# Optimization experiments

Measured on AMD Instinct MI355X. Metric: run time of the kernel, lower is better.

The kernel has to match this reference:

```python
import jax, jax.numpy as jnp
import numpy as np

N_AUTHOR, N_PAPER = 20000, 40000
E = 400000
IN_DIM, HIDDEN, HEADS, NUM_CLASSES, NUM_LAYERS = 128, 128, 8, 16, 2
DIM = HIDDEN // HEADS
NEG_SLOPE = 0.2
AUTHOR_RAW = 64


def setup_inputs() -> dict:
    key = jax.random.key(0)
    ks = jax.random.split(key, 16)
    s = 0.05
    return {
        'x_author': jax.random.normal(ks[0], (N_AUTHOR, AUTHOR_RAW), jnp.float32),
        'x_paper': jax.random.normal(ks[1], (N_PAPER, IN_DIM), jnp.float32),
        'Wa': jax.random.normal(ks[2], (AUTHOR_RAW, IN_DIM), jnp.float32) * s,
        'proj_w': jax.random.normal(ks[3], (NUM_LAYERS, 2, IN_DIM, HIDDEN), jnp.float32) * s,
        'proj_b': jnp.zeros((NUM_LAYERS, 2, HIDDEN), jnp.float32),
        'att_src': jax.random.normal(ks[4], (NUM_LAYERS, 3, HEADS, DIM), jnp.float32) * s,
        'att_dst': jax.random.normal(ks[5], (NUM_LAYERS, 3, HEADS, DIM), jnp.float32) * s,
        'klin_w': jax.random.normal(ks[6], (NUM_LAYERS, HIDDEN, HIDDEN), jnp.float32) * s,
        'klin_b': jnp.zeros((NUM_LAYERS, HIDDEN), jnp.float32),
        'q': jax.random.normal(ks[7], (NUM_LAYERS, HIDDEN), jnp.float32) * s,
        'lin_w': jax.random.normal(ks[8], (HIDDEN, NUM_CLASSES), jnp.float32) * s,
        'lin_b': jnp.zeros((NUM_CLASSES,), jnp.float32),
        'ei_writes': jnp.stack([jax.random.randint(ks[9], (E,), 0, N_AUTHOR),
                                jax.random.randint(ks[10], (E,), 0, N_PAPER)]),
        'ei_written_by': jnp.stack([jax.random.randint(ks[11], (E,), 0, N_PAPER),
                                    jax.random.randint(ks[12], (E,), 0, N_AUTHOR)]),
        'ei_cites': jnp.stack([jax.random.randint(ks[13], (E,), 0, N_PAPER),
                               jax.random.randint(ks[14], (E,), 0, N_PAPER)]),
    }


def _segment_softmax(scores, seg, num_segments):
    # scores: [E, H]; softmax over edges sharing a destination node.
    m = jax.ops.segment_max(scores, seg, num_segments=num_segments)
    m = jnp.where(jnp.isfinite(m), m, 0.0)
    e = jnp.exp(scores - m[seg])
    denom = jax.ops.segment_sum(e, seg, num_segments=num_segments)
    return e / (denom[seg] + 1e-16)


def _han_forward(x_author, x_paper, Wa, proj_w, proj_b, att_src, att_dst,
                 klin_w, klin_b, q, lin_w, lin_b,
                 ei_writes, ei_written_by, ei_cites):
    # Type-alignment projector (author: 64 -> 128, no bias; paper: Identity)
    x = {'author': x_author @ Wa, 'paper': x_paper}
    nsize = {'author': N_AUTHOR, 'paper': N_PAPER}
    ntidx = {'author': 0, 'paper': 1}
    edge_types = [('author', 'paper', ei_writes),
                  ('paper', 'author', ei_written_by),
                  ('paper', 'paper', ei_cites)]
    for l in range(NUM_LAYERS):
        # Per-node-type projection -> [N, H, D]
        xh = {nt: (x[nt] @ proj_w[l, ntidx[nt]] + proj_b[l, ntidx[nt]]).reshape(-1, HEADS, DIM)
              for nt in x}
        outs = {'author': [], 'paper': []}
        for e_id, (src, dst, ei) in enumerate(edge_types):
            a_src = (xh[src] * att_src[l, e_id]).sum(-1)  # [N_src, H]
            a_dst = (xh[dst] * att_dst[l, e_id]).sum(-1)  # [N_dst, H]
            si, di = ei[0], ei[1]
            alpha = a_src[si] + a_dst[di]                 # [E, H]
            alpha = jnp.where(alpha >= 0, alpha, NEG_SLOPE * alpha)  # leaky_relu
            alpha = _segment_softmax(alpha, di, nsize[dst])
            # attention dropout omitted (eval mode)
            msg = (xh[src][si] * alpha[:, :, None]).reshape(-1, HIDDEN)  # [E, HIDDEN]
            agg = jax.ops.segment_sum(msg, di, num_segments=nsize[dst])
            outs[dst].append(jax.nn.relu(agg))
        # Semantic-level attention over metapath embeddings per node type
        newx = {}
        for nt, xs in outs.items():
            stk = jnp.stack(xs)  # [M, N, F]
            score = (q[l] * jnp.tanh(stk @ klin_w[l] + klin_b[l]).mean(axis=1)).sum(-1)  # [M]
            attn = jax.nn.softmax(score)
            newx[nt] = (attn[:, None, None] * stk).sum(0)
        x = newx
        if l < NUM_LAYERS - 1:
            x = {nt: jax.nn.relu(v) for nt, v in x.items()}
            # feature dropout omitted (eval mode)
    return x['paper'] @ lin_w + lin_b  # [N_PAPER, NUM_CLASSES]


def reference(x_author, x_paper, Wa, proj_w, proj_b, att_src, att_dst,
              klin_w, klin_b, q, lin_w, lin_b,
              ei_writes, ei_written_by, ei_cites):
    return _han_forward(x_author, x_paper, Wa, proj_w, proj_b, att_src, att_dst,
                        klin_w, klin_b, q, lin_w, lin_b,
                        ei_writes, ei_written_by, ei_cites)
```

## Files before the change

### kernel.cpp

```cpp
#include <hip/hip_runtime.h>
#include <hip/hip_bf16.h>

typedef __hip_bfloat16 bf16;
typedef __hip_bfloat162 bf162;

#define N_AUTHOR 20000
#define N_PAPER  40000
#define NEDGE    400000
#define HID      128
#define HEADS    8
#define DIMH     16
#define NCLS     16

typedef short short4v __attribute__((ext_vector_type(4)));
typedef short short8v __attribute__((ext_vector_type(8)));
typedef float f32x4   __attribute__((ext_vector_type(4)));

__device__ __forceinline__ bf162 mk2(float a, float b){
    bf162 r; r.x = __float2bfloat16(a); r.y = __float2bfloat16(b); return r;
}

__device__ __forceinline__ float fast_tanh(float x){
    x = fminf(fmaxf(x, -15.f), 15.f);
    float e = __expf(2.f * x);
    return (e - 1.f) / (e + 1.f);
}

template<int KDIM, int EPI>
__device__ __forceinline__ void bgemm_body(
    const bf16* __restrict__ A, const bf16* __restrict__ Wt, const float* __restrict__ Bb,
    bf16* __restrict__ C, const float* __restrict__ qv, float* __restrict__ score,
    int M, int brow, float* red)
{
    const int tid  = threadIdx.x;
    const int lane = tid & 63;
    const int wv   = tid >> 6;
    const int lr   = lane & 15;
    const int quad = lane >> 4;
    const int row0 = brow * 64 + wv * 16;
    const int arow_i = row0 + lr;
    const bool rowok = arow_i < M;
    const bf16* arow = A + (long)arow_i * KDIM;

    short8v afrag[KDIM / 32];
    #pragma unroll
    for (int kc = 0; kc < KDIM / 32; kc++) {
        short8v f = {0,0,0,0,0,0,0,0};
        if (rowok) f = *(const short8v*)(arow + kc * 32 + quad * 8);
        afrag[kc] = f;
    }

    f32x4 acc[8];
    #pragma unroll
    for (int ct = 0; ct < 8; ct++) acc[ct] = (f32x4){0.f, 0.f, 0.f, 0.f};

    #pragma unroll
    for (int ct = 0; ct < 8; ct++) {
        const bf16* wrow = Wt + (long)(ct * 16 + lr) * KDIM + quad * 8;
        #pragma unroll
        for (int kc = 0; kc < KDIM / 32; kc++) {
            short8v bfrag = *(const short8v*)(wrow + kc * 32);
            acc[ct] = __builtin_amdgcn_mfma_f32_16x16x32_bf16(afrag[kc], bfrag, acc[ct], 0, 0, 0);
        }
    }

    if (EPI == 0) {
        #pragma unroll
        for (int ct = 0; ct < 8; ct++) {
            float bc = Bb ? Bb[ct * 16 + lr] : 0.f;
            #pragma unroll
            for (int r = 0; r < 4; r++) {
                int orow = row0 + quad * 4 + r;
                if (orow < M)
                    C[(long)orow * HID + ct * 16 + lr] = __float2bfloat16(acc[ct][r] + bc);
            }
        }
    } else {
        float part = 0.f;
        #pragma unroll
        for (int ct = 0; ct < 8; ct++) {
            float bc = Bb ? Bb[ct * 16 + lr] : 0.f;
            float qc = qv[ct * 16 + lr];
            #pragma unroll
            for (int r = 0; r < 4; r++) {
                int orow = row0 + quad * 4 + r;
                if (orow < M) part += qc * fast_tanh(acc[ct][r] + bc);
            }
        }
        red[tid] = part;
        __syncthreads();
        for (int s = 128; s > 0; s >>= 1) {
            if (tid < s) red[tid] += red[tid + s];
            __syncthreads();
        }
        if (tid == 0) atomicAdd(score, red[0]);
    }
}

template<int KDIM, int EPI>
__global__ __launch_bounds__(256) void bgemm_kernel(
    const bf16* __restrict__ A, const bf16* __restrict__ Wt, const float* __restrict__ Bb,
    bf16* __restrict__ C, const float* __restrict__ qv, float* __restrict__ score, int M)
{
    __shared__ float red[256];
    bgemm_body<KDIM, EPI>(A, Wt, Bb, C, qv, score, M, blockIdx.x, red);
}

template<int KDIM, int EPI>
__global__ __launch_bounds__(256) void bgemm_pair_kernel(
    const bf16* __restrict__ A0, const bf16* __restrict__ Wt0, const float* __restrict__ Bb0,
    bf16* __restrict__ C0, float* __restrict__ score0, int M0, int NB0,
    const bf16* __restrict__ A1, const bf16* __restrict__ Wt1, const float* __restrict__ Bb1,
    bf16* __restrict__ C1, float* __restrict__ score1, int M1,
    const float* __restrict__ qv)
{
    __shared__ float red[256];
    const int bx = blockIdx.x;
    if (bx < NB0)
        bgemm_body<KDIM, EPI>(A0, Wt0, Bb0, C0, qv, score0, M0, bx, red);
    else
        bgemm_body<KDIM, EPI>(A1, Wt1, Bb1, C1, qv, score1, M1, bx - NB0, red);
}

#define R_WA  (128 * 64)
#define R_PW  (4 * 128 * 128)
#define R_KW  (2 * 128 * 128)

__global__ void conv_weights_kernel(const float* __restrict__ Wa,
                                    const float* __restrict__ proj_w,
                                    const float* __restrict__ klin_w,
                                    bf16* __restrict__ wt_wa,
                                    bf16* __restrict__ wt_proj,
                                    bf16* __restrict__ wt_klin)
{
    int i = blockIdx.x * blockDim.x + threadIdx.x;
    if (i < R_WA) {
        int n = i >> 6, k = i & 63;
        wt_wa[i] = __float2bfloat16(Wa[k * 128 + n]);
    } else if (i < R_WA + R_PW) {
        int j = i - R_WA;
        int m = j >> 14, r = j & 16383;
        int n = r >> 7, k = r & 127;
        wt_proj[j] = __float2bfloat16(proj_w[m * 16384 + k * 128 + n]);
    } else if (i < R_WA + R_PW + R_KW) {
        int j = i - R_WA - R_PW;
        int m = j >> 14, r = j & 16383;
        int n = r >> 7, k = r & 127;
        wt_klin[j] = __float2bfloat16(klin_w[m * 16384 + k * 128 + n]);
    }
}

#define NXA (N_AUTHOR * 64)
#define NXP (N_PAPER * HID)

__global__ void conv_x_kernel(const float* __restrict__ xa_f, const float* __restrict__ xp_f,
                              bf16* __restrict__ xa, bf16* __restrict__ xp)
{
    int i4 = blockIdx.x * blockDim.x + threadIdx.x;
    int i = i4 * 4;
    if (i < NXA) {
        float4 v = *(const float4*)(xa_f + i);
        xa[i]   = __float2bfloat16(v.x); xa[i+1] = __float2bfloat16(v.y);
        xa[i+2] = __float2bfloat16(v.z); xa[i+3] = __float2bfloat16(v.w);
    } else if (i < NXA + NXP) {
        int j = i - NXA;
        float4 v = *(const float4*)(xp_f + j);
        xp[j]   = __float2bfloat16(v.x); xp[j+1] = __float2bfloat16(v.y);
        xp[j+2] = __float2bfloat16(v.z); xp[j+3] = __float2bfloat16(v.w);
    }
}

__global__ void node_att_multi_kernel(const bf16* __restrict__ xh,
    const float* __restrict__ A0, const float* __restrict__ A1,
    const float* __restrict__ A2, const float* __restrict__ A3,
    float* __restrict__ O0, float* __restrict__ O1,
    float* __restrict__ O2, float* __restrict__ O3, int N)
{
    int i = blockIdx.x * blockDim.x + threadIdx.x;
    if (i >= N * HEADS) return;
    int n = i >> 3, h = i & 7;
    const bf16* row = xh + (long)n * HID + h * DIMH;
    float x[DIMH];
    #pragma unroll
    for (int d = 0; d < DIMH; d++) x[d] = __bfloat162float(row[d]);
    if (A0) { float s = 0.f;
        #pragma unroll
        for (int d = 0; d < DIMH; d++) s += x[d] * A0[h*DIMH + d];
        O0[i] = s; }
    if (A1) { float s = 0.f;
        #pragma unroll
        for (int d = 0; d < DIMH; d++) s += x[d] * A1[h*DIMH + d];
        O1[i] = s; }
    if (A2) { float s = 0.f;
        #pragma unroll
        for (int d = 0; d < DIMH; d++) s += x[d] * A2[h*DIMH + d];
        O2[i] = s; }
    if (A3) { float s = 0.f;
        #pragma unroll
        for (int d = 0; d < DIMH; d++) s += x[d] * A3[h*DIMH + d];
        O3[i] = s; }
}

#define CNT_OFF1 N_PAPER
#define CNT_OFF2 (N_PAPER + N_AUTHOR)

__global__ void hist3_kernel(const int* __restrict__ d0, const int* __restrict__ d1,
                             const int* __restrict__ d2, int* __restrict__ cnt,
                             unsigned short* __restrict__ rank)
{
    int i = blockIdx.x * blockDim.x + threadIdx.x;
    if (i < NEDGE)               rank[i] = (unsigned short)atomicAdd(&cnt[d0[i]], 1);
    else if (i < 2*NEDGE)        rank[i] = (unsigned short)atomicAdd(&cnt[CNT_OFF1 + d1[i - NEDGE]], 1);
    else if (i < 3*NEDGE)        rank[i] = (unsigned short)atomicAdd(&cnt[CNT_OFF2 + d2[i - 2*NEDGE]], 1);
}

__device__ __forceinline__ int job_nd(int j){ return j == 1 ? N_AUTHOR : N_PAPER; }
__device__ __forceinline__ int job_off(int j){ return j == 0 ? 0 : (j == 1 ? CNT_OFF1 : CNT_OFF2); }

__global__ __launch_bounds__(256) void scan_a3_kernel(const int* __restrict__ cnt,
                                                      int* __restrict__ bsum)
{
    int j = blockIdx.y;
    int nd = job_nd(j), off = job_off(j);
    __shared__ int s[256];
    int tid = threadIdx.x;
    int i = blockIdx.x * 256 + tid;
    s[tid] = (i < nd) ? cnt[off + i] : 0;
    __syncthreads();
    for (int st = 128; st > 0; st >>= 1) {
        if (tid < st) s[tid] += s[tid + st];
        __syncthreads();
    }
    if (tid == 0) bsum[j * 256 + blockIdx.x] = s[0];
}

__global__ __launch_bounds__(256) void scan_b3_kernel(int* __restrict__ bsum,
    int* __restrict__ roff0, int* __restrict__ roff1, int* __restrict__ roff2)
{
    int j = blockIdx.x;
    int nd = job_nd(j);
    int nb = (nd + 255) / 256;
    int* roff = j == 0 ? roff0 : (j == 1 ? roff1 : roff2);
    __shared__ int s[256];
    int tid = threadIdx.x;
    int v = (tid < nb) ? bsum[j * 256 + tid] : 0;
    s[tid] = v;
    __syncthreads();
    for (int off = 1; off < 256; off <<= 1) {
        int t = (tid >= off) ? s[tid - off] : 0;
        __syncthreads();
        s[tid] += t;
        __syncthreads();
    }
    if (tid < nb) bsum[j * 256 + tid] = s[tid] - v;
    if (tid == 255) roff[nd] = s[255];
}

__global__ __launch_bounds__(256) void scan_c3_kernel(const int* __restrict__ cnt,
    const int* __restrict__ bsum,
    int* __restrict__ roff0, int* __restrict__ roff1, int* __restrict__ roff2)
{
    int j = blockIdx.y;
    int nd = job_nd(j), off = job_off(j);
    int* roff = j == 0 ? roff0 : (j == 1 ? roff1 : roff2);
    __shared__ int s[256];
    int tid = threadIdx.x;
    int i = blockIdx.x * 256 + tid;
    int v = (i < nd) ? cnt[off + i] : 0;
    s[tid] = v;
    __syncthreads();
    for (int o = 1; o < 256; o <<= 1) {
        int t = (tid >= o) ? s[tid - o] : 0;
        __syncthreads();
        s[tid] += t;
        __syncthreads();
    }
    if (i < nd) roff[i] = bsum[j * 256 + blockIdx.x] + s[tid] - v;
}

__global__ void fill3_kernel(
    const int* __restrict__ s0, const int* __restrict__ d0,
    const int* __restrict__ s1, const int* __restrict__ d1,
    const int* __restrict__ s2, const int* __restrict__ d2,
    const int* __restrict__ roff0, const int* __restrict__ roff1, const int* __restrict__ roff2,
    const unsigned short* __restrict__ rank,
    unsigned short* __restrict__ c0, unsigned short* __restrict__ c1, unsigned short* __restrict__ c2)
{
    int i = blockIdx.x * blockDim.x + threadIdx.x;
    if (i < NEDGE) {
        int d = d0[i];
        c0[roff0[d] + rank[i]] = (unsigned short)s0[i];
    } else if (i < 2*NEDGE) {
        int e = i - NEDGE, d = d1[e];
        c1[roff1[d] + rank[i]] = (unsigned short)s1[e];
    } else if (i < 3*NEDGE) {
        int e = i - 2*NEDGE, d = d2[e];
        c2[roff2[d] + rank[i]] = (unsigned short)s2[e];
    }
}

__global__ __launch_bounds__(256) void paper_gather2_kernel(
    const int* __restrict__ roff0, const unsigned short* __restrict__ csrc0,
    const float* __restrict__ as0, const float* __restrict__ ad0,
    const bf16* __restrict__ xha,
    const int* __restrict__ roff2, const unsigned short* __restrict__ csrc2,
    const float* __restrict__ as2, const float* __restrict__ ad2,
    const bf16* __restrict__ xhp,
    bf16* __restrict__ out0, bf16* __restrict__ out2)
{
    int w = blockIdx.x * 4 + (threadIdx.x >> 6);
    int lane = threadIdx.x & 63;
    if (w >= N_PAPER) return;
    int h = lane >> 3;
    int b0 = roff0[w], n0 = roff0[w + 1] - b0;
    int b2 = roff2[w], n2 = roff2[w + 1] - b2;
    float ad0v = ad0[(long)w * 8 + h];
    float ad2v = ad2[(long)w * 8 + h];
    float den0 = 0.f, p00 = 0.f, p01 = 0.f;
    float den2 = 0.f, p20 = 0.f, p21 = 0.f;
    int nmax = n0 > n2 ? n0 : n2;
    int c0m = n0 > 0 ? n0 - 1 : 0;
    int c2m = n2 > 0 ? n2 - 1 : 0;
    for (int i = 0; i < nmax; i += 8) {
        int sA[8], sB[8];
        #pragma unroll
        for (int u = 0; u < 8; u++) {
            sA[u] = csrc0[b0 + min(i + u, c0m)];
            sB[u] = csrc2[b2 + min(i + u, c2m)];
        }
        float aA[8], aB[8];
        bf162 xA[8], xB[8];
        #pragma unroll
        for (int u = 0; u < 8; u++) {
            aA[u] = as0[(long)sA[u] * 8 + h];
            xA[u] = *(const bf162*)(xha + (long)sA[u] * HID + lane * 2);
            aB[u] = as2[(long)sB[u] * 8 + h];
            xB[u] = *(const bf162*)(xhp + (long)sB[u] * HID + lane * 2);
        }
        #pragma unroll
        for (int u = 0; u < 8; u++) {
            float a = aA[u] + ad0v;
            a = a >= 0.f ? a : 0.2f * a;
            float wt = __expf(fminf(a, 60.f));
            wt = (i + u < n0) ? wt : 0.f;
            den0 += wt;
            p00 = fmaf(__bfloat162float(xA[u].x), wt, p00);
            p01 = fmaf(__bfloat162float(xA[u].y), wt, p01);
            a = aB[u] + ad2v;
            a = a >= 0.f ? a : 0.2f * a;
            wt = __expf(fminf(a, 60.f));
            wt = (i + u < n2) ? wt : 0.f;
            den2 += wt;
            p20 = fmaf(__bfloat162float(xB[u].x), wt, p20);
            p21 = fmaf(__bfloat162float(xB[u].y), wt, p21);
        }
    }
    float inv0 = 1.f / (den0 + 1e-16f);
    float inv2 = 1.f / (den2 + 1e-16f);
    *(bf162*)(out0 + (long)w * HID + lane * 2) = mk2(fmaxf(p00 * inv0, 0.f), fmaxf(p01 * inv0, 0.f));
    *(bf162*)(out2 + (long)w * HID + lane * 2) = mk2(fmaxf(p20 * inv2, 0.f), fmaxf(p21 * inv2, 0.f));
}

__global__ __launch_bounds__(256) void edge_gather_kernel(
    const int* __restrict__ roff, const unsigned short* __restrict__ csrc,
    const float* __restrict__ as_, const float* __restrict__ ad_,
    const bf16* __restrict__ xh, bf16* __restrict__ out, int Ndst)
{
    int w = blockIdx.x * 4 + (threadIdx.x >> 6);
    int lane = threadIdx.x & 63;
    if (w >= Ndst) return;
    int h = lane >> 3;
    int beg = roff[w], n = roff[w + 1] - beg;
    float ad = ad_[(long)w * 8 + h];
    float den = 0.f, acc0 = 0.f, acc1 = 0.f;
    int cm = n > 0 ? n - 1 : 0;
    for (int i = 0; i < n; i += 8) {
        int s[8];
        #pragma unroll
        for (int u = 0; u < 8; u++) s[u] = csrc[beg + min(i + u, cm)];
        float av[8]; bf162 xv[8];
        #pragma unroll
        for (int u = 0; u < 8; u++) {
            av[u] = as_[(long)s[u] * 8 + h];
            xv[u] = *(const bf162*)(xh + (long)s[u] * HID + lane * 2);
        }
        #pragma unroll
        for (int u = 0; u < 8; u++) {
            float a = av[u] + ad;
            a = a >= 0.f ? a : 0.2f * a;
            float wt = __expf(fminf(a, 60.f));
            wt = (i + u < n) ? wt : 0.f;
            den += wt;
            acc0 = fmaf(__bfloat162float(xv[u].x), wt, acc0);
            acc1 = fmaf(__bfloat162float(xv[u].y), wt, acc1);
        }
    }
    float inv = 1.f / (den + 1e-16f);
    *(bf162*)(out + (long)w * HID + lane * 2) = mk2(fmaxf(acc0 * inv, 0.f), fmaxf(acc1 * inv, 0.f));
}

__global__ void combine_kernel(const bf16* __restrict__ a0, const bf16* __restrict__ a1,
                               const float* __restrict__ score, bf16* __restrict__ out, int n2)
{
    int i = blockIdx.x * blockDim.x + threadIdx.x;
    if (i >= n2) return;
    float s0 = score[0] * (1.f / N_PAPER);
    float s1 = score[1] * (1.f / N_PAPER);
    float m = fmaxf(s0, s1);
    float e0 = __expf(s0 - m), e1 = __expf(s1 - m);
    float inv = 1.f / (e0 + e1);
    float w0 = e0 * inv, w1 = e1 * inv;
    bf162 v0 = ((const bf162*)a0)[i];
    bf162 v1 = ((const bf162*)a1)[i];
    ((bf162*)out)[i] = mk2(w0 * __bfloat162float(v0.x) + w1 * __bfloat162float(v1.x),
                           w0 * __bfloat162float(v0.y) + w1 * __bfloat162float(v1.y));
}

__global__ __launch_bounds__(256) void final_lin_fused_kernel(
    const bf16* __restrict__ a0, const bf16* __restrict__ a1,
    const float* __restrict__ score,
    const float* __restrict__ W, const float* __restrict__ B, float* __restrict__ out)
{
    __shared__ float Ws[HID * NCLS];
    int tid = threadIdx.x;
    for (int i = tid; i < HID * NCLS; i += 256) Ws[i] = W[i];
    __syncthreads();
    float s0 = score[0] * (1.f / N_PAPER);
    float s1 = score[1] * (1.f / N_PAPER);
    float m = fmaxf(s0, s1);
    float e0 = __expf(s0 - m), e1 = __expf(s1 - m);
    float inv = 1.f / (e0 + e1);
    float w0 = e0 * inv, w1 = e1 * inv;
    int i = blockIdx.x * 256 + tid;
    if (i >= N_PAPER * NCLS) return;
    int n = i >> 4, c = i & 15;
    float acc = B[c];
    const bf16* x0 = a0 + (long)n * HID;
    const bf16* x1 = a1 + (long)n * HID;
    #pragma unroll 16
    for (int k = 0; k < HID; k++)
        acc = fmaf(fmaf(w0, __bfloat162float(x0[k]), w1 * __bfloat162float(x1[k])),
                   Ws[k * NCLS + c], acc);
    out[i] = acc;
}

extern "C" void kernel_launch(void* const* d_in, const int* in_sizes, int n_in,
                              void* d_out, int out_size, void* d_ws, size_t ws_size,
                              hipStream_t stream)
{
    const float* x_author = (const float*)d_in[0];
    const float* x_paper  = (const float*)d_in[1];
    const float* Wa       = (const float*)d_in[2];
    const float* proj_w   = (const float*)d_in[3];
    const float* proj_b   = (const float*)d_in[4];
    const float* att_src  = (const float*)d_in[5];
    const float* att_dst  = (const float*)d_in[6];
    const float* klin_w   = (const float*)d_in[7];
    const float* klin_b   = (const float*)d_in[8];
    const float* qv       = (const float*)d_in[9];
    const float* lin_w    = (const float*)d_in[10];
    const float* lin_b    = (const float*)d_in[11];
    const int*  ei_w      = (const int*)d_in[12];
    const int*  ei_wb     = (const int*)d_in[13];
    const int*  ei_c      = (const int*)d_in[14];
    float* out = (float*)d_out;
    (void)ws_size; (void)in_sizes; (void)n_in; (void)out_size;

    char* base = (char*)d_ws;
    size_t off = 0;
    auto alloc = [&](size_t bytes) {
        void* p = base + off;
        off = (off + bytes + 255) & ~(size_t)255;
        return p;
    };
    bf16*  xh_a  = (bf16*) alloc((size_t)N_AUTHOR * HID * 2);
    bf16*  xh_p  = (bf16*) alloc((size_t)N_PAPER  * HID * 2);
    bf16*  buf_a = (bf16*) alloc((size_t)N_AUTHOR * HID * 2);
    bf16*  buf_p = (bf16*) alloc((size_t)N_PAPER  * HID * 2);
    bf16*  agg_p1= (bf16*) alloc((size_t)N_PAPER  * HID * 2);
    bf16*  xa    = (bf16*) alloc((size_t)N_AUTHOR * 64  * 2);
    bf16*  xp    = (bf16*) alloc((size_t)N_PAPER  * HID * 2);
    bf16*  wt_wa   = (bf16*)alloc((size_t)R_WA * 2);
    bf16*  wt_proj = (bf16*)alloc((size_t)R_PW * 2);
    bf16*  wt_klin = (bf16*)alloc((size_t)R_KW * 2);
    float* a_e0s = (float*)alloc((size_t)N_AUTHOR * HEADS * 4);
    float* a_e0d = (float*)alloc((size_t)N_PAPER  * HEADS * 4);
    float* a_e1s = (float*)alloc((size_t)N_PAPER  * HEADS * 4);
    float* a_e1d = (float*)alloc((size_t)N_AUTHOR * HEADS * 4);
    float* a_e2s = (float*)alloc((size_t)N_PAPER  * HEADS * 4);
    float* a_e2d = (float*)alloc((size_t)N_PAPER  * HEADS * 4);
    float* score  = (float*)alloc(64);
    int* roff0 = (int*)alloc((size_t)(N_PAPER  + 1) * 4);
    int* roff1 = (int*)alloc((size_t)(N_AUTHOR + 1) * 4);
    int* roff2 = (int*)alloc((size_t)(N_PAPER  + 1) * 4);
    unsigned short* csrc0 = (unsigned short*)alloc((size_t)NEDGE * 2 + 64);
    unsigned short* csrc1 = (unsigned short*)alloc((size_t)NEDGE * 2 + 64);
    unsigned short* csrc2 = (unsigned short*)alloc((size_t)NEDGE * 2 + 64);
    int* cnt   = (int*)alloc((size_t)(2 * N_PAPER + N_AUTHOR) * 4);
    unsigned short* rank = (unsigned short*)alloc((size_t)(3 * NEDGE) * 2);
    int* bsum  = (int*)alloc(3 * 256 * 4);

    const int GA = (N_AUTHOR + 63) / 64;
    const int GP = (N_PAPER  + 63) / 64;
    const int G3E = (3 * NEDGE + 255) / 256;
    const int NBMAX = (N_PAPER + 255) / 256;

    conv_weights_kernel<<<(R_WA + R_PW + R_KW + 255)/256, 256, 0, stream>>>(
        Wa, proj_w, klin_w, wt_wa, wt_proj, wt_klin);
    conv_x_kernel<<<((NXA + NXP)/4 + 255)/256, 256, 0, stream>>>(x_author, x_paper, xa, xp);

    hipMemsetAsync(cnt, 0, (size_t)(2 * N_PAPER + N_AUTHOR) * 4, stream);
    hist3_kernel<<<G3E, 256, 0, stream>>>(ei_w + NEDGE, ei_wb + NEDGE, ei_c + NEDGE, cnt, rank);
    scan_a3_kernel<<<dim3(NBMAX, 3), 256, 0, stream>>>(cnt, bsum);
    scan_b3_kernel<<<3, 256, 0, stream>>>(bsum, roff0, roff1, roff2);
    scan_c3_kernel<<<dim3(NBMAX, 3), 256, 0, stream>>>(cnt, bsum, roff0, roff1, roff2);
    fill3_kernel<<<G3E, 256, 0, stream>>>(
        ei_w, ei_w + NEDGE, ei_wb, ei_wb + NEDGE, ei_c, ei_c + NEDGE,
        roff0, roff1, roff2, rank, csrc0, csrc1, csrc2);

    bgemm_kernel<64, 0><<<GA, 256, 0, stream>>>(
        xa, wt_wa, nullptr, buf_a, nullptr, nullptr, N_AUTHOR);

    for (int l = 0; l < 2; l++) {
        const bool last = (l == 1);
        const bf16* cur_a = buf_a;
        const bf16* cur_p = (l == 0) ? xp : buf_p;
        const bf16* pw_a = wt_proj + (size_t)(l*2 + 0) * HID * HID;
        const bf16* pw_p = wt_proj + (size_t)(l*2 + 1) * HID * HID;
        const float* pb_a = proj_b + (size_t)(l*2 + 0) * HID;
        const float* pb_p = proj_b + (size_t)(l*2 + 1) * HID;

        bgemm_pair_kernel<128, 0><<<GA + GP, 256, 0, stream>>>(
            cur_a, pw_a, pb_a, xh_a, nullptr, N_AUTHOR, GA,
            cur_p, pw_p, pb_p, xh_p, nullptr, N_PAPER, nullptr);

        hipMemsetAsync(score, 0, 64, stream);

        const float* as0 = att_src + (size_t)(l*3 + 0) * HID;
        const float* ad0 = att_dst + (size_t)(l*3 + 0) * HID;
        const float* as1 = att_src + (size_t)(l*3 + 1) * HID;
        const float* ad1 = att_dst + (size_t)(l*3 + 1) * HID;
        const float* as2 = att_src + (size_t)(l*3 + 2) * HID;
        const float* ad2 = att_dst + (size_t)(l*3 + 2) * HID;

        node_att_multi_kernel<<<(N_AUTHOR*HEADS + 255)/256, 256, 0, stream>>>(
            xh_a, as0, last ? nullptr : ad1, nullptr, nullptr,
            a_e0s, a_e1d, nullptr, nullptr, N_AUTHOR);
        node_att_multi_kernel<<<(N_PAPER*HEADS + 255)/256, 256, 0, stream>>>(
            xh_p, ad0, last ? nullptr : as1, as2, ad2,
            a_e0d, a_e1s, a_e2s, a_e2d, N_PAPER);

        paper_gather2_kernel<<<(N_PAPER + 3)/4, 256, 0, stream>>>(
            roff0, csrc0, a_e0s, a_e0d, xh_a,
            roff2, csrc2, a_e2s, a_e2d, xh_p,
            buf_p, agg_p1);
        if (!last)
            edge_gather_kernel<<<(N_AUTHOR + 3)/4, 256, 0, stream>>>(
                roff1, csrc1, a_e1s, a_e1d, xh_p, buf_a, N_AUTHOR);

        const bf16* kw = wt_klin + (size_t)l * HID * HID;
        const float* kb = klin_b + (size_t)l * HID;
        const float* qq = qv     + (size_t)l * HID;
        bgemm_pair_kernel<128, 1><<<2 * GP, 256, 0, stream>>>(
            buf_p, kw, kb, (bf16*)nullptr, score + 0, N_PAPER, GP,
            agg_p1, kw, kb, (bf16*)nullptr, score + 1, N_PAPER, qq);

        if (!last)
            combine_kernel<<<(N_PAPER*HID/2 + 255)/256, 256, 0, stream>>>(
                buf_p, agg_p1, score, buf_p, N_PAPER*HID/2);
    }

    final_lin_fused_kernel<<<(N_PAPER*NCLS + 255)/256, 256, 0, stream>>>(
        buf_p, agg_p1, score, lin_w, lin_b, out);
}
```

Measured before the change: 480.7 us.

## Widen gather loads to 16B per lane, process four nodes per wavefront

The edge gather kernels now have each 16-lane group handle one destination node, with every lane loading 8 bf16 features as a 16-byte vector. Before, a whole wavefront handled one node using 4-byte loads per lane. This aims to cut the number of memory instructions per gathered row and raise the number of nodes in flight. Each lane now keeps 8 accumulators, which adds register pressure. The change also reorders the GEMM inner loop to batch the weight-fragment loads ahead of the MFMAs, and swaps divisions for hardware reciprocal calls, including in tanh.

```diff
diff --git a/kernel.cpp b/kernel.cpp
--- a/kernel.cpp
+++ b/kernel.cpp
@@ -19,11 +19,20 @@
 __device__ __forceinline__ bf162 mk2(float a, float b){
     bf162 r; r.x = __float2bfloat16(a); r.y = __float2bfloat16(b); return r;
 }
+__device__ __forceinline__ float b2f(short s){
+    return __uint_as_float(((unsigned)(unsigned short)s) << 16);
+}
+__device__ __forceinline__ short f2bs(float v){
+    unsigned u = __float_as_uint(v);
+    unsigned r = (u + 0x7FFFu + ((u >> 16) & 1u)) >> 16;
+    return (short)r;
+}
+__device__ __forceinline__ float fastrcp(float x){ return __builtin_amdgcn_rcpf(x); }
 
 __device__ __forceinline__ float fast_tanh(float x){
     x = fminf(fmaxf(x, -15.f), 15.f);
     float e = __expf(2.f * x);
-    return (e - 1.f) / (e + 1.f);
+    return 1.f - 2.f * fastrcp(e + 1.f);
 }
 
 template<int KDIM, int EPI>
@@ -55,13 +64,14 @@
     for (int ct = 0; ct < 8; ct++) acc[ct] = (f32x4){0.f, 0.f, 0.f, 0.f};
 
     #pragma unroll
-    for (int ct = 0; ct < 8; ct++) {
-        const bf16* wrow = Wt + (long)(ct * 16 + lr) * KDIM + quad * 8;
-        #pragma unroll
-        for (int kc = 0; kc < KDIM / 32; kc++) {
-            short8v bfrag = *(const short8v*)(wrow + kc * 32);
-            acc[ct] = __builtin_amdgcn_mfma_f32_16x16x32_bf16(afrag[kc], bfrag, acc[ct], 0, 0, 0);
-        }
+    for (int kc = 0; kc < KDIM / 32; kc++) {
+        short8v bfrag[8];
+        #pragma unroll
+        for (int ct = 0; ct < 8; ct++)
+            bfrag[ct] = *(const short8v*)(Wt + (long)(ct * 16 + lr) * KDIM + kc * 32 + quad * 8);
+        #pragma unroll
+        for (int ct = 0; ct < 8; ct++)
+            acc[ct] = __builtin_amdgcn_mfma_f32_16x16x32_bf16(afrag[kc], bfrag[ct], acc[ct], 0, 0, 0);
     }
 
     if (EPI == 0) {
@@ -308,57 +318,71 @@
     const bf16* __restrict__ xhp,
     bf16* __restrict__ out0, bf16* __restrict__ out2)
 {
-    int w = blockIdx.x * 4 + (threadIdx.x >> 6);
     int lane = threadIdx.x & 63;
+    int li   = lane & 15;
+    int sub  = lane >> 4;
+    int w = blockIdx.x * 16 + (threadIdx.x >> 6) * 4 + sub;
     if (w >= N_PAPER) return;
-    int h = lane >> 3;
+    int h = li >> 1;
+
     int b0 = roff0[w], n0 = roff0[w + 1] - b0;
     int b2 = roff2[w], n2 = roff2[w + 1] - b2;
     float ad0v = ad0[(long)w * 8 + h];
     float ad2v = ad2[(long)w * 8 + h];
-    float den0 = 0.f, p00 = 0.f, p01 = 0.f;
-    float den2 = 0.f, p20 = 0.f, p21 = 0.f;
+    float den0 = 0.f, den2 = 0.f;
+    float acc0[8], acc2[8];
+    #pragma unroll
+    for (int j = 0; j < 8; j++) { acc0[j] = 0.f; acc2[j] = 0.f; }
+
     int nmax = n0 > n2 ? n0 : n2;
     int c0m = n0 > 0 ? n0 - 1 : 0;
     int c2m = n2 > 0 ? n2 - 1 : 0;
-    for (int i = 0; i < nmax; i += 8) {
-        int sA[8], sB[8];
-        #pragma unroll
-        for (int u = 0; u < 8; u++) {
+    for (int i = 0; i < nmax; i += 4) {
+        int sA[4], sB[4];
+        #pragma unroll
+        for (int u = 0; u < 4; u++) {
             sA[u] = csrc0[b0 + min(i + u, c0m)];
             sB[u] = csrc2[b2 + min(i + u, c2m)];
         }
-        float aA[8], aB[8];
-        bf162 xA[8], xB[8];
-        #pragma unroll
-        for (int u = 0; u < 8; u++) {
+        float aA[4], aB[4];
+        short8v xA[4], xB[4];
+        #pragma unroll
+        for (int u = 0; u < 4; u++) {
             aA[u] = as0[(long)sA[u] * 8 + h];
-            xA[u] = *(const bf162*)(xha + (long)sA[u] * HID + lane * 2);
+            xA[u] = *(const short8v*)(xha + (long)sA[u] * HID + li * 8);
             aB[u] = as2[(long)sB[u] * 8 + h];
-            xB[u] = *(const bf162*)(xhp + (long)sB[u] * HID + lane * 2);
-        }
-        #pragma unroll
-        for (int u = 0; u < 8; u++) {
+            xB[u] = *(const short8v*)(xhp + (long)sB[u] * HID + li * 8);
+        }
+        #pragma unroll
+        for (int u = 0; u < 4; u++) {
             float a = aA[u] + ad0v;
             a = a >= 0.f ? a : 0.2f * a;
             float wt = __expf(fminf(a, 60.f));
             wt = (i + u < n0) ? wt : 0.f;
             den0 += wt;
-            p00 = fmaf(__bfloat162float(xA[u].x), wt, p00);
-            p01 = fmaf(__bfloat162float(xA[u].y), wt, p01);
+            #pragma unroll
+            for (int j = 0; j < 8; j++)
+                acc0[j] = fmaf(b2f(xA[u][j]), wt, acc0[j]);
             a = aB[u] + ad2v;
             a = a >= 0.f ? a : 0.2f * a;
             wt = __expf(fminf(a, 60.f));
             wt = (i + u < n2) ? wt : 0.f;
             den2 += wt;
-            p20 = fmaf(__bfloat162float(xB[u].x), wt, p20);
-            p21 = fmaf(__bfloat162float(xB[u].y), wt, p21);
-        }
-    }
-    float inv0 = 1.f / (den0 + 1e-16f);
-    float inv2 = 1.f / (den2 + 1e-16f);
-    *(bf162*)(out0 + (long)w * HID + lane * 2) = mk2(fmaxf(p00 * inv0, 0.f), fmaxf(p01 * inv0, 0.f));
-    *(bf162*)(out2 + (long)w * HID + lane * 2) = mk2(fmaxf(p20 * inv2, 0.f), fmaxf(p21 * inv2, 0.f));
+            #pragma unroll
+            for (int j = 0; j < 8; j++)
+                acc2[j] = fmaf(b2f(xB[u][j]), wt, acc2[j]);
+        }
+    }
+    float inv0 = fastrcp(den0 + 1e-16f);
+    float inv2 = fastrcp(den2 + 1e-16f);
+    short8v o0, o2;
+    #pragma unroll
+    for (int j = 0; j < 8; j++) {
+        o0[j] = f2bs(fmaxf(acc0[j] * inv0, 0.f));
+        o2[j] = f2bs(fmaxf(acc2[j] * inv2, 0.f));
+    }
+    *(short8v*)(out0 + (long)w * HID + li * 8) = o0;
+    *(short8v*)(out2 + (long)w * HID + li * 8) = o2;
 }
 
 __global__ __launch_bounds__(256) void edge_gather_kernel(
@@ -366,37 +390,46 @@
     const float* __restrict__ as_, const float* __restrict__ ad_,
     const bf16* __restrict__ xh, bf16* __restrict__ out, int Ndst)
 {
-    int w = blockIdx.x * 4 + (threadIdx.x >> 6);
     int lane = threadIdx.x & 63;
+    int li   = lane & 15;
+    int sub  = lane >> 4;
+    int w = blockIdx.x * 16 + (threadIdx.x >> 6) * 4 + sub;
     if (w >= Ndst) return;
-    int h = lane >> 3;
+    int h = li >> 1;
     int beg = roff[w], n = roff[w + 1] - beg;
-    float ad = ad_[(long)w * 8 + h];
-    float den = 0.f, acc0 = 0.f, acc1 = 0.f;
+    float adv = ad_[(long)w * 8 + h];
+    float den = 0.f;
+    float acc[8];
+    #pragma unroll
+    for (int j = 0; j < 8; j++) acc[j] = 0.f;
     int cm = n > 0 ? n - 1 : 0;
-    for (int i = 0; i < n; i += 8) {
-        int s[8];
-        #pragma unroll
-        for (int u = 0; u < 8; u++) s[u] = csrc[beg + min(i + u, cm)];
-        float av[8]; bf162 xv[8];
-        #pragma unroll
-        for (int u = 0; u < 8; u++) {
+    for (int i = 0; i < n; i += 4) {
+        int s[4];
+        #pragma unroll
+        for (int u = 0; u < 4; u++) s[u] = csrc[beg + min(i + u, cm)];
+        float av[4]; short8v xv[4];
+        #pragma unroll
+        for (int u = 0; u < 4; u++) {
             av[u] = as_[(long)s[u] * 8 + h];
-            xv[u] = *(const bf162*)(xh + (long)s[u] * HID + lane * 2);
-        }
-        #pragma unroll
-        for (int u = 0; u < 8; u++) {
-            float a = av[u] + ad;
+            xv[u] = *(const short8v*)(xh + (long)s[u] * HID + li * 8);
+        }
+        #pragma unroll
+        for (int u = 0; u < 4; u++) {
+            float a = av[u] + adv;
             a = a >= 0.f ? a : 0.2f * a;
             float wt = __expf(fminf(a, 60.f));
             wt = (i + u < n) ? wt : 0.f;
             den += wt;
-            acc0 = fmaf(__bfloat162float(xv[u].x), wt, acc0);
-            acc1 = fmaf(__bfloat162float(xv[u].y), wt, acc1);
-        }
-    }
-    float inv = 1.f / (den + 1e-16f);
-    *(bf162*)(out + (long)w * HID + lane * 2) = mk2(fmaxf(acc0 * inv, 0.f), fmaxf(acc1 * inv, 0.f));
+            #pragma unroll
+            for (int j = 0; j < 8; j++)
+                acc[j] = fmaf(b2f(xv[u][j]), wt, acc[j]);
+        }
+    }
+    float inv = fastrcp(den + 1e-16f);
+    short8v o;
+    #pragma unroll
+    for (int j = 0; j < 8; j++) o[j] = f2bs(fmaxf(acc[j] * inv, 0.f));
+    *(short8v*)(out + (long)w * HID + li * 8) = o;
 }
 
 __global__ void combine_kernel(const bf16* __restrict__ a0, const bf16* __restrict__ a1,
@@ -408,7 +441,7 @@
     float s1 = score[1] * (1.f / N_PAPER);
     float m = fmaxf(s0, s1);
     float e0 = __expf(s0 - m), e1 = __expf(s1 - m);
-    float inv = 1.f / (e0 + e1);
+    float inv = fastrcp(e0 + e1);
     float w0 = e0 * inv, w1 = e1 * inv;
     bf162 v0 = ((const bf162*)a0)[i];
     bf162 v1 = ((const bf162*)a1)[i];
@@ -550,12 +583,12 @@
             xh_p, ad0, last ? nullptr : as1, as2, ad2,
             a_e0d, a_e1s, a_e2s, a_e2d, N_PAPER);
 
-        paper_gather2_kernel<<<(N_PAPER + 3)/4, 256, 0, stream>>>(
+        paper_gather2_kernel<<<(N_PAPER + 15)/16, 256, 0, stream>>>(
             roff0, csrc0, a_e0s, a_e0d, xh_a,
             roff2, csrc2, a_e2s, a_e2d, xh_p,
             buf_p, agg_p1);
         if (!last)
-            edge_gather_kernel<<<(N_AUTHOR + 3)/4, 256, 0, stream>>>(
+            edge_gather_kernel<<<(N_AUTHOR + 15)/16, 256, 0, stream>>>(
                 roff1, csrc1, a_e1s, a_e1d, xh_p, buf_a, N_AUTHOR);
 
         const bf16* kw = wt_klin + (size_t)l * HID * HID;
```

After: 451.2 us. 1.07x faster.
